# Optimization experiments

Hardware: AMD Instinct MI355X
Metric: run time of the kernel (lower is better)

Reference implementation:

```python
import jax, jax.numpy as jnp
import numpy as np

N = 50000   # nodes
E = 300000  # edges (before self-loops)
G = 128     # graphs in batch
H = 4       # heads
C = 64      # hidden channels per head
IN = 32     # input node features
HC = H * C  # 256


def setup_inputs() -> dict:
    key = jax.random.key(0)
    ks = jax.random.split(key, 64)
    p = lambda k, s, sc=0.1: sc * jax.random.normal(k, s, dtype=jnp.float32)
    d = {}
    d['x'] = jax.random.normal(ks[0], (N, IN), dtype=jnp.float32)
    d['edge_attr'] = jax.random.uniform(ks[1], (E, 1), dtype=jnp.float32)
    i = 2
    dims = [(IN, HC), (HC, HC), (HC, HC)]
    for l, (din, dout) in enumerate(dims):
        d[f'w{l}'] = p(ks[i], (din, dout)); i += 1
        d[f'as{l}'] = p(ks[i], (H, C)); i += 1
        d[f'ad{l}'] = p(ks[i], (H, C)); i += 1
        d[f'we{l}'] = p(ks[i], (1, dout)); i += 1
        d[f'ae{l}'] = p(ks[i], (H, C)); i += 1
    d['b0'] = jnp.zeros((HC,), jnp.float32)
    d['b1'] = jnp.zeros((HC,), jnp.float32)
    d['b2'] = jnp.zeros((C,), jnp.float32)
    for l, n in [(0, HC), (1, HC), (2, C)]:
        d[f'bn_g{l}'] = jnp.ones((n,), jnp.float32)
        d[f'bn_b{l}'] = jnp.zeros((n,), jnp.float32)
        d[f'bn_m{l}'] = p(ks[i], (n,), 0.01); i += 1
        d[f'bn_v{l}'] = jnp.ones((n,), jnp.float32)
    d['emb'] = p(ks[i], (1000, 16)); i += 1
    d['mw1'] = p(ks[i], (2 * C + 16, 128)); i += 1
    d['mb1'] = jnp.zeros((128,), jnp.float32)
    d['mw2'] = p(ks[i], (128, 64)); i += 1
    d['mb2'] = jnp.zeros((64,), jnp.float32)
    d['mw3'] = p(ks[i], (64, 2)); i += 1
    d['mb3'] = jnp.zeros((2,), jnp.float32)
    d['edge_index'] = jax.random.randint(ks[i], (2, E), 0, N); i += 1
    d['batch'] = jnp.sort(jax.random.randint(ks[i], (N,), 0, G)); i += 1
    d['circuit_ids'] = jax.random.randint(ks[i], (G,), 0, 1000)
    return d


def _gat(x, src, dst, ea, W, a_s, a_d, We, a_e, b, concat):
    # PyG GATConv (v1): shared lin for src/dst, per-edge attention with edge features,
    # segment softmax over incoming edges of each destination node.
    h = (x @ W).reshape(N, H, C)              # [N,H,C]
    ee = (ea @ We).reshape(-1, H, C)          # [E',H,C]
    alpha = (h * a_s).sum(-1)[src] + (h * a_d).sum(-1)[dst] + (ee * a_e).sum(-1)  # [E',H]
    alpha = jax.nn.leaky_relu(alpha, 0.2)
    m = jax.ops.segment_max(alpha, dst, num_segments=N)
    w = jnp.exp(alpha - m[dst])
    den = jax.ops.segment_sum(w, dst, num_segments=N)
    att = w / den[dst]                        # [E',H]
    out = jax.ops.segment_sum(h[src] * att[:, :, None], dst, num_segments=N)  # [N,H,C]
    return out.reshape(N, HC) + b if concat else out.mean(axis=1) + b


def _bn(x, g, b, m, v):
    # eval-mode BatchNorm1d with materialized running stats
    return (x - m) * jax.lax.rsqrt(v + 1e-5) * g + b


def reference(x, edge_attr,
              w0, as0, ad0, we0, ae0,
              w1, as1, ad1, we1, ae1,
              w2, as2, ad2, we2, ae2,
              b0, b1, b2,
              bn_g0, bn_b0, bn_m0, bn_v0,
              bn_g1, bn_b1, bn_m1, bn_v1,
              bn_g2, bn_b2, bn_m2, bn_v2,
              emb, mw1, mb1, mw2, mb2, mw3, mb3,
              edge_index, batch, circuit_ids):
    loop = jnp.arange(N)
    src = jnp.concatenate([edge_index[0], loop])
    dst = jnp.concatenate([edge_index[1], loop])
    # PyG add_self_loops with fill_value='mean' for edge_attr
    ea = jnp.concatenate([edge_attr, jnp.broadcast_to(edge_attr.mean(axis=0, keepdims=True), (N, 1))], axis=0)

    h = _gat(x, src, dst, ea, w0, as0, ad0, we0, ae0, b0, True)
    h = jax.nn.elu(_bn(h, bn_g0, bn_b0, bn_m0, bn_v0))
    h = _gat(h, src, dst, ea, w1, as1, ad1, we1, ae1, b1, True)
    h = jax.nn.elu(_bn(h, bn_g1, bn_b1, bn_m1, bn_v1))
    h = _gat(h, src, dst, ea, w2, as2, ad2, we2, ae2, b2, False)
    h = _bn(h, bn_g2, bn_b2, bn_m2, bn_v2)

    cnt = jnp.maximum(jax.ops.segment_sum(jnp.ones((N,), h.dtype), batch, num_segments=G), 1.0)
    xmean = jax.ops.segment_sum(h, batch, num_segments=G) / cnt[:, None]
    xmax = jax.ops.segment_max(h, batch, num_segments=G)
    gfeat = jnp.concatenate([xmean, xmax], axis=1)          # [G, 2*C]
    comb = jnp.concatenate([gfeat, emb[circuit_ids]], axis=1)  # [G, 2*C+16]
    z = jax.nn.relu(comb @ mw1 + mb1)
    z = jax.nn.relu(z @ mw2 + mb2)
    return z @ mw3 + mb3
```

## Files before the change

kernel.cpp:

```cpp
#include <hip/hip_runtime.h>
#include <cmath>

#define DEV static __device__ __forceinline__

typedef _Float16 half8 __attribute__((ext_vector_type(8)));
typedef _Float16 half4 __attribute__((ext_vector_type(4)));
typedef float f32x4 __attribute__((ext_vector_type(4)));

DEV float warp64_sum(float v) {
    for (int o = 32; o > 0; o >>= 1) v += __shfl_xor(v, o, 64);
    return v;
}

DEV unsigned fkey(float f) {
    unsigned b = __float_as_uint(f);
    return (b & 0x80000000u) ? ~b : (b | 0x80000000u);
}
DEV float fdecode(unsigned k) {
    return (k & 0x80000000u) ? __uint_as_float(k ^ 0x80000000u) : __uint_as_float(~k);
}

__global__ __launch_bounds__(256) void k_count(const int* __restrict__ ei,
                                               const float* __restrict__ ea,
                                               int* __restrict__ cnt,
                                               float* __restrict__ easum, int E, int Nn) {
    __shared__ float ls[4];
    float s = 0.f;
    int total = E + Nn;
    for (int i = blockIdx.x * blockDim.x + threadIdx.x; i < total; i += gridDim.x * blockDim.x) {
        int d;
        if (i < E) { d = ei[E + i]; s += ea[i]; }
        else       d = i - E;
        atomicAdd(&cnt[d], 1);
    }
    s = warp64_sum(s);
    int lane = threadIdx.x & 63, w = threadIdx.x >> 6;
    if (lane == 0) ls[w] = s;
    __syncthreads();
    if (threadIdx.x == 0) {
        float t = ls[0] + ls[1] + ls[2] + ls[3];
        if (t != 0.f) atomicAdd(easum, t);
    }
}

__global__ __launch_bounds__(256) void k_scan1(const int* __restrict__ counts,
                                               int* __restrict__ offs,
                                               int* __restrict__ bsum, int n) {
    __shared__ int ls[256];
    int t = threadIdx.x;
    int base = blockIdx.x * 1024 + t * 4;
    int4 v = {0, 0, 0, 0};
    if (base + 3 < n) v = *(const int4*)&counts[base];
    else {
        if (base + 0 < n) v.x = counts[base + 0];
        if (base + 1 < n) v.y = counts[base + 1];
        if (base + 2 < n) v.z = counts[base + 2];
    }
    int s = v.x + v.y + v.z + v.w;
    ls[t] = s;
    __syncthreads();
    for (int o = 1; o < 256; o <<= 1) {
        int u = (t >= o) ? ls[t - o] : 0;
        __syncthreads();
        ls[t] += u;
        __syncthreads();
    }
    if (t == 255) bsum[blockIdx.x] = ls[255];
    int o0 = ls[t] - s;
    int o1 = o0 + v.x, o2 = o1 + v.y, o3 = o2 + v.z;
    if (base + 3 < n) { *(int4*)&offs[base] = make_int4(o0, o1, o2, o3); }
    else {
        if (base + 0 < n) offs[base + 0] = o0;
        if (base + 1 < n) offs[base + 1] = o1;
        if (base + 2 < n) offs[base + 2] = o2;
    }
}

__global__ __launch_bounds__(256) void k_scan2(int* __restrict__ bsum,
                                               int* __restrict__ offs, int nb,
                                               int total, int n) {
    __shared__ int ls[256];
    int t = threadIdx.x;
    int s = (t < nb) ? bsum[t] : 0;
    ls[t] = s;
    __syncthreads();
    for (int o = 1; o < 256; o <<= 1) {
        int u = (t >= o) ? ls[t - o] : 0;
        __syncthreads();
        ls[t] += u;
        __syncthreads();
    }
    if (t < nb) bsum[t] = ls[t] - s;
    if (t == 0) offs[n] = total;
}

__global__ __launch_bounds__(256) void k_scan3(int* __restrict__ offs,
                                               const int* __restrict__ bsum, int n) {
    int add = bsum[blockIdx.x];
    if (add == 0) return;
    int i = blockIdx.x * 1024 + threadIdx.x * 4;
    if (i + 3 < n) {
        int4 v = *(int4*)&offs[i];
        v.x += add; v.y += add; v.z += add; v.w += add;
        *(int4*)&offs[i] = v;
    } else {
        for (int j = 0; j < 4 && i + j < n; ++j) offs[i + j] += add;
    }
}

__global__ void k_scatter(const int* __restrict__ ei, const float* __restrict__ ea,
                          const float* __restrict__ easum, const int* __restrict__ offs,
                          int* __restrict__ cur, int* __restrict__ csrc,
                          float* __restrict__ cea, int E, int Nn) {
    float eam = easum[0] / (float)E;
    int total = E + Nn;
    for (int i = blockIdx.x * blockDim.x + threadIdx.x; i < total; i += gridDim.x * blockDim.x) {
        int s, d; float v;
        if (i < E) { s = ei[i]; d = ei[E + i]; v = ea[i]; }
        else       { s = d = i - E; v = eam; }
        int pos = offs[d] + atomicAdd(&cur[d], 1);
        csrc[pos] = s;
        cea[pos] = v;
    }
}

__global__ __launch_bounds__(256) void k_coef(const float* __restrict__ we0, const float* __restrict__ ae0,
                                              const float* __restrict__ we1, const float* __restrict__ ae1,
                                              const float* __restrict__ we2, const float* __restrict__ ae2,
                                              float* __restrict__ coef) {
    int t = threadIdx.x, h = t >> 6, lane = t & 63;
    const float* we[3] = {we0, we1, we2};
    const float* ae[3] = {ae0, ae1, ae2};
#pragma unroll
    for (int l = 0; l < 3; ++l) {
        float p = we[l][t] * ae[l][t];
        p = warp64_sum(p);
        if (lane == 0) coef[l * 4 + h] = p;
    }
}

__global__ __launch_bounds__(256) void k_prep(
    const float* __restrict__ b0, const float* __restrict__ g0, const float* __restrict__ be0,
    const float* __restrict__ m0, const float* __restrict__ v0,
    const float* __restrict__ b1, const float* __restrict__ g1, const float* __restrict__ be1,
    const float* __restrict__ m1, const float* __restrict__ v1,
    const float* __restrict__ b2, const float* __restrict__ g2, const float* __restrict__ be2,
    const float* __restrict__ m2, const float* __restrict__ v2,
    float* __restrict__ sAB) {
    int t = threadIdx.x;
    {
        float rs = rsqrtf(v0[t] + 1e-5f) * g0[t];
        sAB[t] = rs;
        sAB[256 + t] = (b0[t] - m0[t]) * rs + be0[t];
    }
    {
        float rs = rsqrtf(v1[t] + 1e-5f) * g1[t];
        sAB[512 + t] = rs;
        sAB[768 + t] = (b1[t] - m1[t]) * rs + be1[t];
    }
    if (t < 64) {
        float rs = rsqrtf(v2[t] + 1e-5f) * g2[t];
        sAB[1024 + t] = rs;
        sAB[1088 + t] = (b2[t] - m2[t]) * rs + be2[t];
    }
}

__global__ __launch_bounds__(256) void k_cvt_x(const float* __restrict__ x,
                                               _Float16* __restrict__ xh,
                                               int nvalid_rows, int cols, int total) {
    int i = blockIdx.x * 256 + threadIdx.x;
    if (i >= total) return;
    int r = i / cols;
    xh[i] = (r < nvalid_rows) ? (_Float16)x[i] : (_Float16)0.f;
}

__global__ __launch_bounds__(256) void k_cvt_w3(const float* __restrict__ w0,
                                                const float* __restrict__ w1,
                                                const float* __restrict__ w2,
                                                _Float16* __restrict__ wt0,
                                                _Float16* __restrict__ wt1,
                                                _Float16* __restrict__ wt2) {
    const int S0 = 256 * 32, S1 = 256 * 256;
    int i = blockIdx.x * 256 + threadIdx.x;
    if (i < S0) {
        int c = i / 32, k = i - c * 32;
        wt0[i] = (_Float16)w0[k * 256 + c];
    } else if (i < S0 + S1) {
        int j = i - S0;
        int c = j / 256, k = j - c * 256;
        wt1[j] = (_Float16)w1[k * 256 + c];
    } else if (i < S0 + 2 * S1) {
        int j = i - S0 - S1;
        int c = j / 256, k = j - c * 256;
        wt2[j] = (_Float16)w2[k * 256 + c];
    }
}

template <int KT>
__global__ __launch_bounds__(256) void k_gemm_mfma(const _Float16* __restrict__ A,
                                                   const _Float16* __restrict__ Wt,
                                                   _Float16* __restrict__ Out, int nrows,
                                                   const float* __restrict__ as_,
                                                   const float* __restrict__ ad_,
                                                   float* __restrict__ ssrc,
                                                   float* __restrict__ sdst) {
    constexpr int STRIDE = KT + 8;
    __shared__ _Float16 As[64 * STRIDE];
    const int tid = threadIdx.x;
    const int lane = tid & 63, wc = tid >> 6;
    const int l15 = lane & 15, g = lane >> 4;
    const int row0 = blockIdx.x * 64;

    {
        constexpr int CPR = KT / 8;
        constexpr int CHUNKS = 64 * CPR;
#pragma unroll
        for (int c = tid; c < CHUNKS; c += 256) {
            int r = c / CPR;
            int kc = (c - r * CPR) * 8;
            half8 v = *(const half8*)(A + (size_t)(row0 + r) * KT + kc);
            *(half8*)(As + r * STRIDE + kc) = v;
        }
    }
    __syncthreads();

    f32x4 acc[4][4] = {};
    const _Float16* Wb = Wt + (size_t)(wc * 64 + l15) * KT + g * 8;
    const _Float16* Ab = As + l15 * STRIDE + g * 8;

#pragma unroll
    for (int kk = 0; kk < KT; kk += 32) {
        half8 af[4], bf[4];
#pragma unroll
        for (int m = 0; m < 4; ++m)
            af[m] = *(const half8*)(Ab + m * 16 * STRIDE + kk);
#pragma unroll
        for (int f = 0; f < 4; ++f)
            bf[f] = *(const half8*)(Wb + (size_t)f * 16 * KT + kk);
#pragma unroll
        for (int m = 0; m < 4; ++m)
#pragma unroll
            for (int f = 0; f < 4; ++f)
                acc[m][f] = __builtin_amdgcn_mfma_f32_16x16x32_f16(af[m], bf[f], acc[m][f], 0, 0, 0);
    }

    float asv[4], adv[4];
#pragma unroll
    for (int f = 0; f < 4; ++f) {
        asv[f] = as_[wc * 64 + f * 16 + l15];
        adv[f] = ad_[wc * 64 + f * 16 + l15];
    }

#pragma unroll
    for (int m = 0; m < 4; ++m) {
        float ps[4] = {}, pd[4] = {};
#pragma unroll
        for (int f = 0; f < 4; ++f)
#pragma unroll
            for (int j = 0; j < 4; ++j) {
                ps[j] = fmaf(acc[m][f][j], asv[f], ps[j]);
                pd[j] = fmaf(acc[m][f][j], adv[f], pd[j]);
            }
#pragma unroll
        for (int o = 1; o < 16; o <<= 1)
#pragma unroll
            for (int j = 0; j < 4; ++j) {
                ps[j] += __shfl_xor(ps[j], o, 64);
                pd[j] += __shfl_xor(pd[j], o, 64);
            }
        if (l15 == 0) {
#pragma unroll
            for (int j = 0; j < 4; ++j) {
                int r = row0 + m * 16 + g * 4 + j;
                if (r < nrows) {
                    ssrc[r * 4 + wc] = ps[j];
                    sdst[r * 4 + wc] = pd[j];
                }
            }
        }
#pragma unroll
        for (int f = 0; f < 4; ++f)
#pragma unroll
            for (int j = 0; j < 4; ++j) {
                int r = row0 + m * 16 + g * 4 + j;
                if (r < nrows)
                    Out[(size_t)r * 256 + wc * 64 + f * 16 + l15] = (_Float16)acc[m][f][j];
            }
    }
}

template <bool MEAN>
__global__ __launch_bounds__(256) void k_agg(const _Float16* __restrict__ hlin,
                                             const int* __restrict__ offs,
                                             const int* __restrict__ csrc,
                                             const float* __restrict__ cea,
                                             const float* __restrict__ ssrc,
                                             const float* __restrict__ sdst,
                                             const float* __restrict__ coef,
                                             const float* __restrict__ sA,
                                             const float* __restrict__ sB,
                                             _Float16* __restrict__ outh,
                                             float* __restrict__ outf, int Nn) {
    int n = blockIdx.x * 4 + (threadIdx.x >> 6);
    if (n >= Nn) return;
    int lane = threadIdx.x & 63;
    int h = lane >> 4, s = lane & 15;
    int b = offs[n], e = offs[n + 1];
    int deg = e - b;
    float sd = sdst[n * 4 + h], cf = coef[h];
    const _Float16* hrow = hlin + lane * 4;

    f32x4 acc = {};
    float inv;

    if (deg <= 16) {
        float a0 = -INFINITY;
        if (s < deg) {
            int i = b + s;
            float a = ssrc[csrc[i] * 4 + h] + sd + cf * cea[i];
            a0 = a > 0.f ? a : 0.2f * a;
        }
        float m = a0;
#pragma unroll
        for (int o = 1; o < 16; o <<= 1) m = fmaxf(m, __shfl_xor(m, o, 64));
        float p = (s < deg) ? __expf(a0 - m) : 0.f;
        float den = p;
#pragma unroll
        for (int o = 1; o < 16; o <<= 1) den += __shfl_xor(den, o, 64);
        inv = 1.f / den;

        {
            half4 hv[8];
#pragma unroll
            for (int k = 0; k < 8; ++k) {
                int kc = k < deg ? k : deg - 1;
                hv[k] = *(const half4*)(hrow + (size_t)csrc[b + kc] * 256);
            }
#pragma unroll
            for (int k = 0; k < 8; ++k) {
                float pk = __shfl(p, (h << 4) | k, 64);
#pragma unroll
                for (int j = 0; j < 4; ++j) acc[j] = fmaf(pk, (float)hv[k][j], acc[j]);
            }
        }
        if (deg > 8) {
            half4 hv[8];
#pragma unroll
            for (int k = 0; k < 8; ++k) {
                int kk = 8 + k;
                int kc = kk < deg ? kk : deg - 1;
                hv[k] = *(const half4*)(hrow + (size_t)csrc[b + kc] * 256);
            }
#pragma unroll
            for (int k = 0; k < 8; ++k) {
                float pk = __shfl(p, (h << 4) | (8 + k), 64);
#pragma unroll
                for (int j = 0; j < 4; ++j) acc[j] = fmaf(pk, (float)hv[k][j], acc[j]);
            }
        }
    } else {
        float m = -INFINITY, den = 0.f;
        for (int i = b; i < e; ++i) {
            int sn = csrc[i];
            float a = ssrc[sn * 4 + h] + sd + cf * cea[i];
            a = a > 0.f ? a : 0.2f * a;
            float mn = fmaxf(m, a);
            float sc = __expf(m - mn);
            float p = __expf(a - mn);
            den = den * sc + p;
            half4 hv = *(const half4*)(hrow + (size_t)sn * 256);
#pragma unroll
            for (int j = 0; j < 4; ++j) acc[j] = acc[j] * sc + p * (float)hv[j];
            m = mn;
        }
        inv = 1.f / den;
    }

    if (!MEAN) {
        int c = lane * 4;
        float4 a4 = *(const float4*)&sA[c];
        float4 b4 = *(const float4*)&sB[c];
        half4 o;
#pragma unroll
        for (int j = 0; j < 4; ++j) {
            float v = acc[j] * inv * (&a4.x)[j] + (&b4.x)[j];
            v = v > 0.f ? v : expm1f(v);
            o[j] = (_Float16)v;
        }
        *(half4*)(outh + (size_t)n * 256 + c) = o;
    } else {
        float r[4];
#pragma unroll
        for (int j = 0; j < 4; ++j) {
            r[j] = acc[j] * inv;
            r[j] += __shfl_xor(r[j], 16, 64);
            r[j] += __shfl_xor(r[j], 32, 64);
        }
        if (lane < 16) {
            int c = lane * 4;
#pragma unroll
            for (int j = 0; j < 4; ++j) {
                float v = 0.25f * r[j] * sA[c + j] + sB[c + j];
                outf[(size_t)n * 64 + c + j] = v;
            }
        }
    }
}

__global__ __launch_bounds__(256) void k_pool(const float* __restrict__ h2,
                                              const int* __restrict__ batch,
                                              float* __restrict__ psum,
                                              unsigned* __restrict__ pmaxk,
                                              float* __restrict__ pcnt, int Nn) {
    int wglob = blockIdx.x * 4 + (threadIdx.x >> 6);
    int lane = threadIdx.x & 63;
    int nwaves = gridDim.x * 4;
    int span = (Nn + nwaves - 1) / nwaves;
    int b = wglob * span, e = min(b + span, Nn);
    if (b >= e) return;
    int curg = batch[b];
    float s = 0.f, mx = -INFINITY;
    float cnt = 0.f;
    for (int i = b; i < e; ++i) {
        int g = batch[i];
        float v = h2[(size_t)i * 64 + lane];
        if (g != curg) {
            atomicAdd(&psum[curg * 64 + lane], s);
            atomicMax(&pmaxk[curg * 64 + lane], fkey(mx));
            if (lane == 0) atomicAdd(&pcnt[curg], cnt);
            s = 0.f; mx = -INFINITY; cnt = 0.f; curg = g;
        }
        s += v; mx = fmaxf(mx, v); cnt += 1.f;
    }
    atomicAdd(&psum[curg * 64 + lane], s);
    atomicMax(&pmaxk[curg * 64 + lane], fkey(mx));
    if (lane == 0) atomicAdd(&pcnt[curg], cnt);
}

__global__ __launch_bounds__(128) void k_mlp(const float* __restrict__ psum,
                                             const unsigned* __restrict__ pmaxk,
                                             const float* __restrict__ pcnt,
                                             const float* __restrict__ emb,
                                             const int* __restrict__ cids,
                                             const float* __restrict__ mw1, const float* __restrict__ mb1,
                                             const float* __restrict__ mw2, const float* __restrict__ mb2,
                                             const float* __restrict__ mw3, const float* __restrict__ mb3,
                                             float* __restrict__ out) {
    __shared__ float comb[144];
    __shared__ float z1[128];
    __shared__ float z2[64];
    int g = blockIdx.x, t = threadIdx.x;
    float cnt = fmaxf(pcnt[g], 1.f);
    if (t < 64) {
        comb[t] = psum[g * 64 + t] / cnt;
        comb[64 + t] = fdecode(pmaxk[g * 64 + t]);
    }
    if (t < 16) comb[128 + t] = emb[cids[g] * 16 + t];
    __syncthreads();
    float a = mb1[t];
    for (int k = 0; k < 144; ++k) a = fmaf(comb[k], mw1[k * 128 + t], a);
    z1[t] = fmaxf(a, 0.f);
    __syncthreads();
    if (t < 64) {
        float a2 = mb2[t];
        for (int k = 0; k < 128; ++k) a2 = fmaf(z1[k], mw2[k * 64 + t], a2);
        z2[t] = fmaxf(a2, 0.f);
    }
    __syncthreads();
    if (t < 2) {
        float a3 = mb3[t];
        for (int k = 0; k < 64; ++k) a3 = fmaf(z2[k], mw3[k * 2 + t], a3);
        out[g * 2 + t] = a3;
    }
}

extern "C" void kernel_launch(void* const* d_in, const int* in_sizes, int n_in,
                              void* d_out, int out_size, void* d_ws, size_t ws_size,
                              hipStream_t stream) {
    const float* x         = (const float*)d_in[0];
    const float* edge_attr = (const float*)d_in[1];
    const float* w0  = (const float*)d_in[2];
    const float* as0 = (const float*)d_in[3];
    const float* ad0 = (const float*)d_in[4];
    const float* we0 = (const float*)d_in[5];
    const float* ae0 = (const float*)d_in[6];
    const float* w1  = (const float*)d_in[7];
    const float* as1 = (const float*)d_in[8];
    const float* ad1 = (const float*)d_in[9];
    const float* we1 = (const float*)d_in[10];
    const float* ae1 = (const float*)d_in[11];
    const float* w2  = (const float*)d_in[12];
    const float* as2 = (const float*)d_in[13];
    const float* ad2 = (const float*)d_in[14];
    const float* we2 = (const float*)d_in[15];
    const float* ae2 = (const float*)d_in[16];
    const float* b0  = (const float*)d_in[17];
    const float* b1  = (const float*)d_in[18];
    const float* b2  = (const float*)d_in[19];
    const float* bn_g0 = (const float*)d_in[20];
    const float* bn_b0 = (const float*)d_in[21];
    const float* bn_m0 = (const float*)d_in[22];
    const float* bn_v0 = (const float*)d_in[23];
    const float* bn_g1 = (const float*)d_in[24];
    const float* bn_b1 = (const float*)d_in[25];
    const float* bn_m1 = (const float*)d_in[26];
    const float* bn_v1 = (const float*)d_in[27];
    const float* bn_g2 = (const float*)d_in[28];
    const float* bn_b2 = (const float*)d_in[29];
    const float* bn_m2 = (const float*)d_in[30];
    const float* bn_v2 = (const float*)d_in[31];
    const float* emb = (const float*)d_in[32];
    const float* mw1 = (const float*)d_in[33];
    const float* mb1 = (const float*)d_in[34];
    const float* mw2 = (const float*)d_in[35];
    const float* mb2 = (const float*)d_in[36];
    const float* mw3 = (const float*)d_in[37];
    const float* mb3 = (const float*)d_in[38];
    const int* edge_index = (const int*)d_in[39];
    const int* batch      = (const int*)d_in[40];
    const int* cids       = (const int*)d_in[41];

    const int N = in_sizes[40];
    const int E = in_sizes[1];
    const int G = in_sizes[41];
    const int EP = E + N;
    const int NB = (N + 63) / 64;
    const int Npad = NB * 64;
    const int NSB = (N + 1023) / 1024;

    size_t off = 0;
    auto alloc = [&](size_t bytes) -> void* {
        void* p = (char*)d_ws + off;
        off += (bytes + 255) & ~(size_t)255;
        return p;
    };
    int*      counts = (int*)alloc((size_t)N * 4);
    int*      cursor = (int*)alloc((size_t)N * 4);
    float*    psum   = (float*)alloc((size_t)G * 64 * 4);
    unsigned* pmaxk  = (unsigned*)alloc((size_t)G * 64 * 4);
    float*    pcnt   = (float*)alloc((size_t)G * 4);
    float*    easum  = (float*)alloc(4);
    size_t zbytes = off;
    int*   offs = (int*)alloc((size_t)(N + 1) * 4);
    int*   bsum = (int*)alloc(256 * 4);
    int*   csrc = (int*)alloc((size_t)EP * 4);
    float* cea  = (float*)alloc((size_t)EP * 4);
    float* ssrc = (float*)alloc((size_t)N * 4 * 4);
    float* sdst = (float*)alloc((size_t)N * 4 * 4);
    float* coef = (float*)alloc(12 * 4);
    float* sAB  = (float*)alloc(1152 * 4);
    _Float16* xh  = (_Float16*)alloc((size_t)Npad * 32 * 2);
    _Float16* wt0 = (_Float16*)alloc((size_t)256 * 32 * 2);
    _Float16* wt1 = (_Float16*)alloc((size_t)256 * 256 * 2);
    _Float16* wt2 = (_Float16*)alloc((size_t)256 * 256 * 2);
    _Float16* hH  = (_Float16*)alloc((size_t)Npad * 256 * 2);
    _Float16* hB  = (_Float16*)alloc((size_t)Npad * 256 * 2);
    float*    h2  = (float*)alloc((size_t)N * 64 * 4);
    (void)ws_size; (void)n_in; (void)out_size;

    hipMemsetAsync(d_ws, 0, zbytes, stream);

    k_count<<<1024, 256, 0, stream>>>(edge_index, edge_attr, counts, easum, E, N);
    k_scan1<<<NSB, 256, 0, stream>>>(counts, offs, bsum, N);
    k_scan2<<<1, 256, 0, stream>>>(bsum, offs, NSB, EP, N);
    k_scan3<<<NSB, 256, 0, stream>>>(offs, bsum, N);
    k_scatter<<<1024, 256, 0, stream>>>(edge_index, edge_attr, easum, offs, cursor, csrc, cea, E, N);
    k_coef<<<1, 256, 0, stream>>>(we0, ae0, we1, ae1, we2, ae2, coef);
    k_prep<<<1, 256, 0, stream>>>(b0, bn_g0, bn_b0, bn_m0, bn_v0,
                                  b1, bn_g1, bn_b1, bn_m1, bn_v1,
                                  b2, bn_g2, bn_b2, bn_m2, bn_v2, sAB);

    {
        int tot = Npad * 32;
        k_cvt_x<<<(tot + 255) / 256, 256, 0, stream>>>(x, xh, N, 32, tot);
        int wtot = 256 * 32 + 2 * 256 * 256;
        k_cvt_w3<<<(wtot + 255) / 256, 256, 0, stream>>>(w0, w1, w2, wt0, wt1, wt2);
    }

    int agg_grid = (N + 3) / 4;

    k_gemm_mfma<32><<<NB, 256, 0, stream>>>(xh, wt0, hH, N, as0, ad0, ssrc, sdst);
    k_agg<false><<<agg_grid, 256, 0, stream>>>(hH, offs, csrc, cea, ssrc, sdst, coef + 0,
                                               sAB, sAB + 256, hB, nullptr, N);
    k_gemm_mfma<256><<<NB, 256, 0, stream>>>(hB, wt1, hH, N, as1, ad1, ssrc, sdst);
    k_agg<false><<<agg_grid, 256, 0, stream>>>(hH, offs, csrc, cea, ssrc, sdst, coef + 4,
                                               sAB + 512, sAB + 768, hB, nullptr, N);
    k_gemm_mfma<256><<<NB, 256, 0, stream>>>(hB, wt2, hH, N, as2, ad2, ssrc, sdst);
    k_agg<true><<<agg_grid, 256, 0, stream>>>(hH, offs, csrc, cea, ssrc, sdst, coef + 8,
                                              sAB + 1024, sAB + 1088, nullptr, h2, N);

    k_pool<<<512, 256, 0, stream>>>(h2, batch, psum, pmaxk, pcnt, N);
    k_mlp<<<G, 128, 0, stream>>>(psum, pmaxk, pcnt, emb, cids,
                                 mw1, mb1, mw2, mb2, mw3, mb3, (float*)d_out);
}
```

Measured before the change: 282.4 us.

## Aggregate one node per half-wave with 8-channel half8 gathers

The GAT aggregation kernel now handles two destination nodes per 64-lane wave, 32 lanes each. Each lane gathers 8 fp16 channels (16-byte loads) instead of 4, and each lane computes two attention logits so that up to 16 edges are still covered by 8 lanes per head. This doubles per-lane load width and work per wave, cutting the number of load instructions and waves. In exchange it raises register use (8 accumulators, 8 half8 buffers), and the epilogue now reads scale and shift with scalar loads instead of float4.

```diff
diff --git a/kernel.cpp b/kernel.cpp
--- a/kernel.cpp
+++ b/kernel.cpp
@@ -301,61 +301,68 @@
                                              const float* __restrict__ sB,
                                              _Float16* __restrict__ outh,
                                              float* __restrict__ outf, int Nn) {
-    int n = blockIdx.x * 4 + (threadIdx.x >> 6);
+    int n = blockIdx.x * 8 + (threadIdx.x >> 5);
     if (n >= Nn) return;
-    int lane = threadIdx.x & 63;
-    int h = lane >> 4, s = lane & 15;
+    int l32 = threadIdx.x & 31;
+    int halfbase = threadIdx.x & 32;
+    int h = l32 >> 3, s = l32 & 7;
     int b = offs[n], e = offs[n + 1];
     int deg = e - b;
     float sd = sdst[n * 4 + h], cf = coef[h];
-    const _Float16* hrow = hlin + lane * 4;
-
-    f32x4 acc = {};
+    const _Float16* hrow = hlin + l32 * 8;
+
+    float acc[8] = {};
     float inv;
 
     if (deg <= 16) {
-        float a0 = -INFINITY;
+        float a0 = -INFINITY, a1 = -INFINITY;
         if (s < deg) {
             int i = b + s;
             float a = ssrc[csrc[i] * 4 + h] + sd + cf * cea[i];
             a0 = a > 0.f ? a : 0.2f * a;
         }
-        float m = a0;
-#pragma unroll
-        for (int o = 1; o < 16; o <<= 1) m = fmaxf(m, __shfl_xor(m, o, 64));
-        float p = (s < deg) ? __expf(a0 - m) : 0.f;
-        float den = p;
-#pragma unroll
-        for (int o = 1; o < 16; o <<= 1) den += __shfl_xor(den, o, 64);
+        if (s + 8 < deg) {
+            int i = b + s + 8;
+            float a = ssrc[csrc[i] * 4 + h] + sd + cf * cea[i];
+            a1 = a > 0.f ? a : 0.2f * a;
+        }
+        float m = fmaxf(a0, a1);
+#pragma unroll
+        for (int o = 1; o < 8; o <<= 1) m = fmaxf(m, __shfl_xor(m, o, 64));
+        float p0 = (s < deg) ? __expf(a0 - m) : 0.f;
+        float p1 = (s + 8 < deg) ? __expf(a1 - m) : 0.f;
+        float den = p0 + p1;
+#pragma unroll
+        for (int o = 1; o < 8; o <<= 1) den += __shfl_xor(den, o, 64);
         inv = 1.f / den;
 
         {
-            half4 hv[8];
+            half8 hv[8];
 #pragma unroll
             for (int k = 0; k < 8; ++k) {
                 int kc = k < deg ? k : deg - 1;
-                hv[k] = *(const half4*)(hrow + (size_t)csrc[b + kc] * 256);
+                hv[k] = *(const half8*)(hrow + (size_t)csrc[b + kc] * 256);
             }
 #pragma unroll
             for (int k = 0; k < 8; ++k) {
-                float pk = __shfl(p, (h << 4) | k, 64);
-#pragma unroll
-                for (int j = 0; j < 4; ++j) acc[j] = fmaf(pk, (float)hv[k][j], acc[j]);
+                float pk = __shfl(p0, halfbase + (h << 3) + k, 64);
+#pragma unroll
+                for (int j = 0; j < 8; ++j) acc[j] = fmaf(pk, (float)hv[k][j], acc[j]);
             }
         }
         if (deg > 8) {
-            half4 hv[8];
+            half8 hv[8];
 #pragma unroll
             for (int k = 0; k < 8; ++k) {
                 int kk = 8 + k;
                 int kc = kk < deg ? kk : deg - 1;
-                hv[k] = *(const half4*)(hrow + (size_t)csrc[b + kc] * 256);
+                hv[k] = *(const half8*)(hrow + (size_t)csrc[b + kc] * 256);
             }
 #pragma unroll
             for (int k = 0; k < 8; ++k) {
-                float pk = __shfl(p, (h << 4) | (8 + k), 64);
-#pragma unroll
-                for (int j = 0; j < 4; ++j) acc[j] = fmaf(pk, (float)hv[k][j], acc[j]);
+                float pk = __shfl(p1, halfbase + (h << 3) + k, 64);
+#pragma unroll
+                for (int j = 0; j < 8; ++j) acc[j] = fmaf(pk, (float)hv[k][j], acc[j]);
             }
         }
     } else {
@@ -368,38 +375,36 @@
             float sc = __expf(m - mn);
             float p = __expf(a - mn);
             den = den * sc + p;
-            half4 hv = *(const half4*)(hrow + (size_t)sn * 256);
-#pragma unroll
-            for (int j = 0; j < 4; ++j) acc[j] = acc[j] * sc + p * (float)hv[j];
+            half8 hv = *(const half8*)(hrow + (size_t)sn * 256);
+#pragma unroll
+            for (int j = 0; j < 8; ++j) acc[j] = acc[j] * sc + p * (float)hv[j];
             m = mn;
         }
         inv = 1.f / den;
     }
 
     if (!MEAN) {
-        int c = lane * 4;
-        float4 a4 = *(const float4*)&sA[c];
-        float4 b4 = *(const float4*)&sB[c];
-        half4 o;
-#pragma unroll
-        for (int j = 0; j < 4; ++j) {
-            float v = acc[j] * inv * (&a4.x)[j] + (&b4.x)[j];
+        int c = l32 * 8;
+        half8 o;
+#pragma unroll
+        for (int j = 0; j < 8; ++j) {
+            float v = acc[j] * inv * sA[c + j] + sB[c + j];
             v = v > 0.f ? v : expm1f(v);
             o[j] = (_Float16)v;
         }
-        *(half4*)(outh + (size_t)n * 256 + c) = o;
+        *(half8*)(outh + (size_t)n * 256 + c) = o;
     } else {
-        float r[4];
-#pragma unroll
-        for (int j = 0; j < 4; ++j) {
+        float r[8];
+#pragma unroll
+        for (int j = 0; j < 8; ++j) {
             r[j] = acc[j] * inv;
+            r[j] += __shfl_xor(r[j], 8, 64);
             r[j] += __shfl_xor(r[j], 16, 64);
-            r[j] += __shfl_xor(r[j], 32, 64);
-        }
-        if (lane < 16) {
-            int c = lane * 4;
-#pragma unroll
-            for (int j = 0; j < 4; ++j) {
+        }
+        if (l32 < 8) {
+            int c = l32 * 8;
+#pragma unroll
+            for (int j = 0; j < 8; ++j) {
                 float v = 0.25f * r[j] * sA[c + j] + sB[c + j];
                 outf[(size_t)n * 64 + c + j] = v;
             }
@@ -577,7 +582,7 @@
         k_cvt_w3<<<(wtot + 255) / 256, 256, 0, stream>>>(w0, w1, w2, wt0, wt1, wt2);
     }
 
-    int agg_grid = (N + 3) / 4;
+    int agg_grid = (N + 7) / 8;
 
     k_gemm_mfma<32><<<NB, 256, 0, stream>>>(xh, wt0, hH, N, as0, ad0, ssrc, sdst);
     k_agg<false><<<agg_grid, 256, 0, stream>>>(hH, offs, csrc, cea, ssrc, sdst, coef + 0,
```

New measurement: 340.8 us. +20.7%, slower.
